# Kernel tuning notes

Hardware: AMD Instinct MI355X
Metric: run time of the kernel (lower is better)

The kernel has to match this reference:

```python
import jax, jax.numpy as jnp
import numpy as np

D, H = 64, 16
B, S = 4, 4096
PI = 3.1415  # constant used verbatim in the original code


def setup_inputs() -> dict:
    key = jax.random.key(0)
    ks = jax.random.split(key, 11)
    inp = {
        'query': jax.random.normal(ks[0], (B, S, D), dtype=jnp.float32),
        'key': jax.random.normal(ks[1], (B, S, D), dtype=jnp.float32),
        'value': jax.random.normal(ks[2], (B, S, D), dtype=jnp.float32),
        'attn_mask': jnp.zeros((1,), dtype=bool),
        # Linear weights stored as (in, out); y = x @ W + b
        'wq_w': jax.random.normal(ks[3], (D, D * H), dtype=jnp.float32) * 0.05,
        'wq_b': jnp.zeros((D * H,), dtype=jnp.float32),
        'wk_w': jax.random.normal(ks[4], (D, D * H), dtype=jnp.float32) * 0.05,
        'wk_b': jnp.zeros((D * H,), dtype=jnp.float32),
        'wv_w': jax.random.normal(ks[5], (D, D * H), dtype=jnp.float32) * 0.05,
        'wv_b': jnp.zeros((D * H,), dtype=jnp.float32),
        'dense_w': jax.random.normal(ks[6], (D * H, D), dtype=jnp.float32) * 0.05,
        'dense_b': jnp.zeros((D,), dtype=jnp.float32),
    }
    return inp


def reference(query, key, value, attn_mask, wq_w, wq_b, wk_w, wk_b, wv_w, wv_b, dense_w, dense_b):
    b, s, _ = query.shape
    # projections -> (B, S, H, D); einsum axis n = heads
    q = (query @ wq_w + wq_b).reshape(b, s, H, D)
    k = (key @ wk_w + wk_b).reshape(b, s, H, D)
    v = (value @ wv_w + wv_b).reshape(b, s, H, D)

    q = jax.nn.elu(q) + 1.0
    k = jax.nn.elu(k) + 1.0

    pos = PI * jnp.arange(s, dtype=query.dtype) / s  # (S,)
    qc_w = jnp.cos(pos)
    qs_w = jnp.sin(pos)
    kc_w = jnp.sin(pos)  # NB: original uses sin for k_cos too (faithful)
    ks_w = jnp.sin(pos)

    q_cos = q * qc_w[None, :, None, None]
    q_sin = q * qs_w[None, :, None, None]
    k_cos = k * kc_w[None, :, None, None]
    k_sin = k * ks_w[None, :, None, None]

    def lin_attn(qf, kf):
        kv = jnp.einsum('bsnx,bsnz->bnxz', kf, v)      # (B,H,D,D)
        return jnp.einsum('bsnx,bnxz->bsnz', qf, kv)   # (B,S,H,D)

    qkv = lin_attn(q, k)
    qkv_cos = lin_attn(q_cos, k_cos)
    qkv_sin = lin_attn(q_sin, k_sin)

    denom = 1.0 / (
        jnp.einsum('bsnd,bnd->bsn', q, k.sum(axis=1))
        + jnp.einsum('bsnd,bnd->bsn', q_cos, k_cos.sum(axis=1))
        + jnp.einsum('bsnd,bnd->bsn', q_sin, k_sin.sum(axis=1))
        + 1e-05
    )

    O = (qkv + qkv_cos + qkv_sin) * denom[..., None]   # (B,S,H,D)
    concat = O.reshape(b, s, H * D)
    return concat @ dense_w + dense_b
```

## Files before the change

kernel.cpp:

```cpp
#include <hip/hip_runtime.h>
#include <math.h>

#define BB 4
#define SS 4096
#define DD 64
#define HH 16
#define PI_C 3.1415f


typedef __attribute__((ext_vector_type(8))) short short8;
typedef __attribute__((ext_vector_type(4))) float f32x4;

#define MFMA(a, b, c) __builtin_amdgcn_mfma_f32_16x16x32_bf16(a, b, c, 0, 0, 0)

__device__ __forceinline__ short f2bf(float f) {
    union { float f; unsigned u; } v; v.f = f;
    unsigned r = v.u + 0x7FFFu + ((v.u >> 16) & 1u);
    return (short)(r >> 16);
}
__device__ __forceinline__ float bf2f(short s) {
    union { unsigned u; float f; } v;
    v.u = ((unsigned)(unsigned short)s) << 16;
    return v.f;
}
__device__ __forceinline__ short8 cvt8(float4 a, float4 b) {
    short8 r;
    r[0] = f2bf(a.x); r[1] = f2bf(a.y); r[2] = f2bf(a.z); r[3] = f2bf(a.w);
    r[4] = f2bf(b.x); r[5] = f2bf(b.y); r[6] = f2bf(b.z); r[7] = f2bf(b.w);
    return r;
}
__device__ __forceinline__ float elu1(float x) { return x > 0.f ? x + 1.f : __expf(x); }
__device__ __forceinline__ void st4(short* p, short a, short b, short c, short d) {
    union { uint2 u; short s[4]; } x;
    x.s[0] = a; x.s[1] = b; x.s[2] = c; x.s[3] = d;
    *reinterpret_cast<uint2*>(p) = x.u;
}

__global__ __launch_bounds__(256) void k_prep(
    const float* __restrict__ wq, const float* __restrict__ wk,
    const float* __restrict__ wv, const float* __restrict__ wd,
    short* __restrict__ dst)
{
    const int h = blockIdx.x, y = blockIdx.y, t = threadIdx.x;
    const float* src = (y == 0) ? wq : (y == 1) ? wk : (y == 2) ? wv : wd;
    const int rs = (y < 3) ? 1024 : 64;
    const size_t srcbase = (y < 3) ? (size_t)(h * 64) : (size_t)(h * 4096);
    short* dm = dst + (size_t)y * 65536 + (size_t)h * 4096;
#pragma unroll
    for (int j = 0; j < 4; ++j) {
        int idx = j * 1024 + t * 4;
        int r = idx >> 6, c = idx & 63;
        float4 v = *reinterpret_cast<const float4*>(src + (size_t)r * rs + srcbase + c);
        dm[(c + 0) * 64 + r] = f2bf(v.x);
        dm[(c + 1) * 64 + r] = f2bf(v.y);
        dm[(c + 2) * 64 + r] = f2bf(v.z);
        dm[(c + 3) * 64 + r] = f2bf(v.w);
    }
}

__global__ __launch_bounds__(256, 2) void k_phase1(
    const float* __restrict__ key, const float* __restrict__ value,
    const float* __restrict__ wk_b, const float* __restrict__ wv_b,
    const short* __restrict__ wkTb, const short* __restrict__ wvTb,
    float* __restrict__ pkv, float* __restrict__ pkvs,
    float* __restrict__ pks)
{
    const int chunk = blockIdx.x, h = blockIdx.y, b = blockIdx.z;
    const int t = threadIdx.x, w = t >> 6, l = t & 63;
    const int lane15 = l & 15, q8 = (l >> 4) * 8, q4 = (l >> 4) * 4;

    __shared__ short kT[2][64 * 72], vT[2][64 * 72], vsT[2][64 * 72];
    __shared__ float ssin[512];
    __shared__ float sbk[64], sbv[64];
    __shared__ float sred[512];

    short8 bkf[2][4], bvf[2][4];
    {
        const short* wkh = wkTb + (size_t)h * 4096;
        const short* wvh = wvTb + (size_t)h * 4096;
#pragma unroll
        for (int kss = 0; kss < 2; ++kss)
#pragma unroll
            for (int nt = 0; nt < 4; ++nt) {
                bkf[kss][nt] = *reinterpret_cast<const short8*>(wkh + (nt * 16 + lane15) * 64 + kss * 32 + q8);
                bvf[kss][nt] = *reinterpret_cast<const short8*>(wvh + (nt * 16 + lane15) * 64 + kss * 32 + q8);
            }
    }
    ssin[t]       = __sinf(PI_C * (float)(chunk * 512 + t)       * (1.f / 4096.f));
    ssin[t + 256] = __sinf(PI_C * (float)(chunk * 512 + t + 256) * (1.f / 4096.f));
    if (t < 64) sbk[t] = wk_b[h * 64 + t];
    else if (t < 128) sbv[t - 64] = wv_b[h * 64 + (t - 64)];

    float4 kf0, kf1, kf2, kf3, vf0, vf1, vf2, vf3;
    {
        const size_t g = ((size_t)b * SS + chunk * 512 + w * 16 + lane15) * 64 + q8;
        kf0 = *reinterpret_cast<const float4*>(key + g);
        kf1 = *reinterpret_cast<const float4*>(key + g + 4);
        kf2 = *reinterpret_cast<const float4*>(key + g + 32);
        kf3 = *reinterpret_cast<const float4*>(key + g + 36);
        vf0 = *reinterpret_cast<const float4*>(value + g);
        vf1 = *reinterpret_cast<const float4*>(value + g + 4);
        vf2 = *reinterpret_cast<const float4*>(value + g + 32);
        vf3 = *reinterpret_cast<const float4*>(value + g + 36);
    }

    f32x4 ckv[4], ckvs[4];
#pragma unroll
    for (int i = 0; i < 4; ++i) {
        ckv[i]  = (f32x4){0.f, 0.f, 0.f, 0.f};
        ckvs[i] = (f32x4){0.f, 0.f, 0.f, 0.f};
    }
    float aks = 0.f, akss = 0.f;

    auto proj_store = [&](int buf, int sbase) {
        f32x4 ckp[4], cvp[4];
#pragma unroll
        for (int i = 0; i < 4; ++i) {
            ckp[i] = (f32x4){0.f, 0.f, 0.f, 0.f};
            cvp[i] = (f32x4){0.f, 0.f, 0.f, 0.f};
        }
        short8 ak0 = cvt8(kf0, kf1), ak1 = cvt8(kf2, kf3);
        short8 av0 = cvt8(vf0, vf1), av1 = cvt8(vf2, vf3);
#pragma unroll
        for (int nt = 0; nt < 4; ++nt) {
            ckp[nt] = MFMA(ak0, bkf[0][nt], ckp[nt]);
            cvp[nt] = MFMA(av0, bvf[0][nt], cvp[nt]);
            ckp[nt] = MFMA(ak1, bkf[1][nt], ckp[nt]);
            cvp[nt] = MFMA(av1, bvf[1][nt], cvp[nt]);
        }
        const int srel = w * 16 + q4;
#pragma unroll
        for (int nt = 0; nt < 4; ++nt) {
            const int x = nt * 16 + lane15;
            const float bk = sbk[x], bv = sbv[x];
            short ek[4], ev[4], es[4];
#pragma unroll
            for (int r = 0; r < 4; ++r) {
                float kk = elu1(ckp[nt][r] + bk);
                float vv = cvp[nt][r] + bv;
                ek[r] = f2bf(kk);
                ev[r] = f2bf(vv);
                es[r] = f2bf(vv * ssin[sbase + srel + r]);
            }
            st4(&kT [buf][x * 72 + srel], ek[0], ek[1], ek[2], ek[3]);
            st4(&vT [buf][x * 72 + srel], ev[0], ev[1], ev[2], ev[3]);
            st4(&vsT[buf][x * 72 + srel], es[0], es[1], es[2], es[3]);
        }
    };

    __syncthreads();
    proj_store(0, 0);
    __syncthreads();

#pragma unroll 1
    for (int it = 0; it < 8; ++it) {
        const int cur = it & 1;
        if (it < 7) {
            const size_t g = ((size_t)b * SS + chunk * 512 + (it + 1) * 64 + w * 16 + lane15) * 64 + q8;
            kf0 = *reinterpret_cast<const float4*>(key + g);
            kf1 = *reinterpret_cast<const float4*>(key + g + 4);
            kf2 = *reinterpret_cast<const float4*>(key + g + 32);
            kf3 = *reinterpret_cast<const float4*>(key + g + 36);
            vf0 = *reinterpret_cast<const float4*>(value + g);
            vf1 = *reinterpret_cast<const float4*>(value + g + 4);
            vf2 = *reinterpret_cast<const float4*>(value + g + 32);
            vf3 = *reinterpret_cast<const float4*>(value + g + 36);
        }
#pragma unroll
        for (int kstep = 0; kstep < 2; ++kstep) {
            const int so = kstep * 32;
            short8 aV  = *reinterpret_cast<const short8*>(&vT [cur][(w * 16 + lane15) * 72 + so + q8]);
            short8 aVS = *reinterpret_cast<const short8*>(&vsT[cur][(w * 16 + lane15) * 72 + so + q8]);
#pragma unroll
            for (int nt = 0; nt < 4; ++nt) {
                short8 bK = *reinterpret_cast<const short8*>(&kT[cur][(nt * 16 + lane15) * 72 + so + q8]);
                ckv[nt]  = MFMA(aV,  bK, ckv[nt]);
                ckvs[nt] = MFMA(aVS, bK, ckvs[nt]);
            }
        }
        {
            const int sbase = it * 64;
            short8 k0 = *reinterpret_cast<const short8*>(&kT[cur][l * 72 + w * 16]);
            short8 k1 = *reinterpret_cast<const short8*>(&kT[cur][l * 72 + w * 16 + 8]);
#pragma unroll
            for (int e = 0; e < 8; ++e) {
                float fa = bf2f(k0[e]), fb = bf2f(k1[e]);
                aks  += fa + fb;
                akss += fa * ssin[sbase + w * 16 + e] + fb * ssin[sbase + w * 16 + 8 + e];
            }
        }
        if (it < 7) proj_store(cur ^ 1, (it + 1) * 64);
        __syncthreads();
    }

    const int bh = b * HH + h;
    const size_t pbase = ((size_t)(chunk * 64) + bh) * 4096;
#pragma unroll
    for (int nt = 0; nt < 4; ++nt) {
        const int x = nt * 16 + lane15;
#pragma unroll
        for (int r = 0; r < 4; ++r) {
            const int z = w * 16 + q4 + r;
            pkv [pbase + z * 64 + x] = ckv[nt][r];
            pkvs[pbase + z * 64 + x] = ckvs[nt][r];
        }
    }
    sred[t] = aks; sred[256 + t] = akss;
    __syncthreads();
    if (t < 64) {
        pks[((size_t)(chunk * 64) + bh) * 128 + t] =
            sred[t] + sred[64 + t] + sred[128 + t] + sred[192 + t];
    } else if (t < 128) {
        int tt = t - 64;
        pks[((size_t)(chunk * 64) + bh) * 128 + t] =
            sred[256 + tt] + sred[320 + tt] + sred[384 + tt] + sred[448 + tt];
    }
}

__global__ __launch_bounds__(256) void k_reduce(
    const float* __restrict__ pkv, const float* __restrict__ pkvs,
    const float* __restrict__ pks,
    short* __restrict__ kvb, short* __restrict__ kvsb,
    float* __restrict__ ksums)
{
    const int blk = blockIdx.x, t = threadIdx.x;
    if (blk < 512) {
        const float* src = (blk < 256) ? pkv : pkvs;
        short* dst = (blk < 256) ? kvb : kvsb;
        const int o4 = (blk & 255) * 256 + t;
        float4 s = make_float4(0.f, 0.f, 0.f, 0.f);
#pragma unroll
        for (int c = 0; c < 8; ++c) {
            float4 v = reinterpret_cast<const float4*>(src + (size_t)c * 262144)[o4];
            s.x += v.x; s.y += v.y; s.z += v.z; s.w += v.w;
        }
        st4(dst + (size_t)o4 * 4, f2bf(s.x), f2bf(s.y), f2bf(s.z), f2bf(s.w));
    } else {
        const int g = (blk - 512) * 256 + t;
        float4 s = make_float4(0.f, 0.f, 0.f, 0.f);
#pragma unroll
        for (int c = 0; c < 8; ++c) {
            float4 v = reinterpret_cast<const float4*>(pks + (size_t)c * 8192)[g];
            s.x += v.x; s.y += v.y; s.z += v.z; s.w += v.w;
        }
        reinterpret_cast<float4*>(ksums)[g] = s;
    }
}

__global__ __launch_bounds__(256, 2) void k_phase2(
    const float* __restrict__ query, const float* __restrict__ wq_b,
    const short* __restrict__ wqTb,
    const short* __restrict__ kvb, const short* __restrict__ kvsb,
    const float* __restrict__ ksums,
    const short* __restrict__ wdTb, const float* __restrict__ dense_b,
    float* __restrict__ out)
{
    const int st = blockIdx.x, b = blockIdx.y;
    const int s0 = st * 32;
    const int t = threadIdx.x, w = t >> 6, l = t & 63;
    const int lane15 = l & 15, q8 = (l >> 4) * 8, q4 = (l >> 4) * 4;

    __shared__ __align__(16) char smem[34816];
    __shared__ float scc[32];
    short* sqin = reinterpret_cast<short*>(smem);
    short* sqp  = reinterpret_cast<short*>(smem) + 2304 * (1 + w);
    short* sOw  = reinterpret_cast<short*>(smem) + 2304 * 5 + 1152 * w;

    {
        const int row = t >> 3, c8 = (t & 7) * 8;
        const float* qp = query + ((size_t)b * SS + s0 + row) * 64 + c8;
        float4 f0 = *reinterpret_cast<const float4*>(qp);
        float4 f1 = *reinterpret_cast<const float4*>(qp + 4);
        *reinterpret_cast<short8*>(&sqin[row * 72 + c8]) = cvt8(f0, f1);
    }
    if (t < 32) {
        float p = PI_C * (float)(s0 + t) * (1.f / 4096.f);
        scc[t] = __cosf(p) + __sinf(p);
    }
    f32x4 cd[2][4];
#pragma unroll
    for (int rt = 0; rt < 2; ++rt)
#pragma unroll
        for (int nt = 0; nt < 4; ++nt) cd[rt][nt] = (f32x4){0.f, 0.f, 0.f, 0.f};
    __syncthreads();

    short8 aq[2][2];
#pragma unroll
    for (int rt = 0; rt < 2; ++rt)
#pragma unroll
        for (int kss = 0; kss < 2; ++kss)
            aq[rt][kss] = *reinterpret_cast<const short8*>(&sqin[(rt * 16 + lane15) * 72 + kss * 32 + q8]);
    const float ccs0 = scc[lane15], ccs1 = scc[16 + lane15];
    const int drow = l >> 1, dxh = (l & 1) * 32;
    const float ccr = scc[drow];

#pragma unroll 1
    for (int i = 0; i < 4; ++i) {
        const int h = (i << 2) | w;
        const size_t bh = (size_t)(b * HH + h);
        const short* wqh = wqTb + (size_t)h * 4096;
        const short* wdh = wdTb + (size_t)h * 4096;
        const short* kv1 = kvb  + bh * 4096;
        const short* kv2 = kvsb + bh * 4096;

        f32x4 cq[2][4];
#pragma unroll
        for (int rt = 0; rt < 2; ++rt)
#pragma unroll
            for (int nt = 0; nt < 4; ++nt) cq[rt][nt] = (f32x4){0.f, 0.f, 0.f, 0.f};
#pragma unroll
        for (int nt = 0; nt < 4; ++nt) {
            short8 b0 = *reinterpret_cast<const short8*>(wqh + (nt * 16 + lane15) * 64 + q8);
            short8 b1 = *reinterpret_cast<const short8*>(wqh + (nt * 16 + lane15) * 64 + 32 + q8);
            cq[0][nt] = MFMA(b0, aq[0][0], cq[0][nt]);
            cq[1][nt] = MFMA(b0, aq[1][0], cq[1][nt]);
            cq[0][nt] = MFMA(b1, aq[0][1], cq[0][nt]);
            cq[1][nt] = MFMA(b1, aq[1][1], cq[1][nt]);
        }
#pragma unroll
        for (int nt = 0; nt < 4; ++nt) {
            float4 bq = *reinterpret_cast<const float4*>(wq_b + h * 64 + nt * 16 + q4);
#pragma unroll
            for (int rt = 0; rt < 2; ++rt) {
                short e0 = f2bf(elu1(cq[rt][nt][0] + bq.x));
                short e1 = f2bf(elu1(cq[rt][nt][1] + bq.y));
                short e2 = f2bf(elu1(cq[rt][nt][2] + bq.z));
                short e3 = f2bf(elu1(cq[rt][nt][3] + bq.w));
                st4(&sqp[(rt * 16 + lane15) * 72 + nt * 16 + q4], e0, e1, e2, e3);
            }
        }

        float invs0, invs1;
        {
            const float* kp = ksums + bh * 128 + dxh;
            float4 A[8], Bv[8];
#pragma unroll
            for (int j = 0; j < 8; ++j) {
                A[j]  = *reinterpret_cast<const float4*>(kp + j * 4);
                Bv[j] = *reinterpret_cast<const float4*>(kp + 64 + j * 4);
            }
            short8 qr[4];
#pragma unroll
            for (int e = 0; e < 4; ++e)
                qr[e] = *reinterpret_cast<const short8*>(&sqp[drow * 72 + dxh + e * 8]);
            float dsum = 0.f;
#pragma unroll
            for (int j4 = 0; j4 < 8; ++j4)
#pragma unroll
                for (int e4 = 0; e4 < 4; ++e4)
                    dsum += bf2f(qr[j4 >> 1][(j4 & 1) * 4 + e4]) * (A[j4][e4] + ccr * Bv[j4][e4]);
            dsum += __shfl_xor(dsum, 1);
            float invd = 1.f / (dsum + 1e-5f);
            invs0 = __shfl(invd, lane15 * 2);
            invs1 = __shfl(invd, (16 + lane15) * 2);
        }

        short8 qf[2][2];
#pragma unroll
        for (int rt = 0; rt < 2; ++rt)
#pragma unroll
            for (int kss = 0; kss < 2; ++kss)
                qf[rt][kss] = *reinterpret_cast<const short8*>(&sqp[(rt * 16 + lane15) * 72 + kss * 32 + q8]);
        f32x4 cv1[2][4], cv2[2][4];
#pragma unroll
        for (int rt = 0; rt < 2; ++rt)
#pragma unroll
            for (int nt = 0; nt < 4; ++nt) {
                cv1[rt][nt] = (f32x4){0.f, 0.f, 0.f, 0.f};
                cv2[rt][nt] = (f32x4){0.f, 0.f, 0.f, 0.f};
            }
#pragma unroll
        for (int nt = 0; nt < 4; ++nt) {
            const short* a1 = kv1 + (nt * 16 + lane15) * 64;
            const short* a2 = kv2 + (nt * 16 + lane15) * 64;
            short8 f10 = *reinterpret_cast<const short8*>(a1 + q8);
            short8 f11 = *reinterpret_cast<const short8*>(a1 + 32 + q8);
            short8 f20 = *reinterpret_cast<const short8*>(a2 + q8);
            short8 f21 = *reinterpret_cast<const short8*>(a2 + 32 + q8);
#pragma unroll
            for (int rt = 0; rt < 2; ++rt) {
                cv1[rt][nt] = MFMA(f10, qf[rt][0], cv1[rt][nt]);
                cv1[rt][nt] = MFMA(f11, qf[rt][1], cv1[rt][nt]);
                cv2[rt][nt] = MFMA(f20, qf[rt][0], cv2[rt][nt]);
                cv2[rt][nt] = MFMA(f21, qf[rt][1], cv2[rt][nt]);
            }
        }
        short8 wdf[4][2];
#pragma unroll
        for (int nt = 0; nt < 4; ++nt)
#pragma unroll
            for (int kss = 0; kss < 2; ++kss)
                wdf[nt][kss] = *reinterpret_cast<const short8*>(wdh + (nt * 16 + lane15) * 64 + kss * 32 + q8);

#pragma unroll
        for (int rt = 0; rt < 2; ++rt) {
            const float ccsr = rt ? ccs1 : ccs0;
            const float invr = rt ? invs1 : invs0;
#pragma unroll
            for (int nt = 0; nt < 4; ++nt) {
                short e0 = f2bf((cv1[rt][nt][0] + ccsr * cv2[rt][nt][0]) * invr);
                short e1 = f2bf((cv1[rt][nt][1] + ccsr * cv2[rt][nt][1]) * invr);
                short e2 = f2bf((cv1[rt][nt][2] + ccsr * cv2[rt][nt][2]) * invr);
                short e3 = f2bf((cv1[rt][nt][3] + ccsr * cv2[rt][nt][3]) * invr);
                st4(&sOw[lane15 * 72 + nt * 16 + q4], e0, e1, e2, e3);
            }
            short8 of0 = *reinterpret_cast<const short8*>(&sOw[lane15 * 72 + q8]);
            short8 of1 = *reinterpret_cast<const short8*>(&sOw[lane15 * 72 + 32 + q8]);
#pragma unroll
            for (int nt = 0; nt < 4; ++nt) {
                cd[rt][nt] = MFMA(of0, wdf[nt][0], cd[rt][nt]);
                cd[rt][nt] = MFMA(of1, wdf[nt][1], cd[rt][nt]);
            }
        }
    }

    __syncthreads();
    {
        float* red = reinterpret_cast<float*>(smem) + 2176 * w;
#pragma unroll
        for (int rt = 0; rt < 2; ++rt)
#pragma unroll
            for (int nt = 0; nt < 4; ++nt)
#pragma unroll
                for (int r = 0; r < 4; ++r)
                    red[(rt * 16 + q4 + r) * 68 + nt * 16 + lane15] = cd[rt][nt][r];
    }
    __syncthreads();
    {
        const int row = t >> 3, c8 = (t & 7) * 8;
        float4 sa = make_float4(0.f, 0.f, 0.f, 0.f);
        float4 sb = make_float4(0.f, 0.f, 0.f, 0.f);
#pragma unroll
        for (int ww = 0; ww < 4; ++ww) {
            const float* red = reinterpret_cast<const float*>(smem) + 2176 * ww;
            float4 v0 = *reinterpret_cast<const float4*>(red + row * 68 + c8);
            float4 v1 = *reinterpret_cast<const float4*>(red + row * 68 + c8 + 4);
            sa.x += v0.x; sa.y += v0.y; sa.z += v0.z; sa.w += v0.w;
            sb.x += v1.x; sb.y += v1.y; sb.z += v1.z; sb.w += v1.w;
        }
        float4 d0 = *reinterpret_cast<const float4*>(dense_b + c8);
        float4 d1 = *reinterpret_cast<const float4*>(dense_b + c8 + 4);
        sa.x += d0.x; sa.y += d0.y; sa.z += d0.z; sa.w += d0.w;
        sb.x += d1.x; sb.y += d1.y; sb.z += d1.z; sb.w += d1.w;
        float* op = out + ((size_t)b * SS + s0 + row) * 64 + c8;
        *reinterpret_cast<float4*>(op)     = sa;
        *reinterpret_cast<float4*>(op + 4) = sb;
    }
}

extern "C" void kernel_launch(void* const* d_in, const int* in_sizes, int n_in,
                              void* d_out, int out_size, void* d_ws, size_t ws_size,
                              hipStream_t stream) {
    const float* query   = (const float*)d_in[0];
    const float* key     = (const float*)d_in[1];
    const float* value   = (const float*)d_in[2];
    const float* wq_w    = (const float*)d_in[4];
    const float* wq_b    = (const float*)d_in[5];
    const float* wk_w    = (const float*)d_in[6];
    const float* wk_b    = (const float*)d_in[7];
    const float* wv_w    = (const float*)d_in[8];
    const float* wv_b    = (const float*)d_in[9];
    const float* dense_w = (const float*)d_in[10];
    const float* dense_b = (const float*)d_in[11];
    float* out = (float*)d_out;

    char* ws = (char*)d_ws;
    float* pkv   = (float*)(ws);
    float* pkvs  = (float*)(ws + 8388608);
    float* pks   = (float*)(ws + 16777216);
    short* kvb   = (short*)(ws + 17039360);
    short* kvsb  = (short*)(ws + 17563648);
    float* ksums = (float*)(ws + 18087936);
    short* wT    = (short*)(ws + 18120704);
    short* wqTb  = wT;
    short* wkTb  = wT + 65536;
    short* wvTb  = wT + 131072;
    short* wdTb  = wT + 196608;

    hipLaunchKernelGGL(k_prep, dim3(16, 4), dim3(256), 0, stream,
                       wq_w, wk_w, wv_w, dense_w, wT);
    hipLaunchKernelGGL(k_phase1, dim3(8, HH, BB), dim3(256), 0, stream,
                       key, value, wk_b, wv_b, wkTb, wvTb, pkv, pkvs, pks);
    hipLaunchKernelGGL(k_reduce, dim3(520), dim3(256), 0, stream,
                       pkv, pkvs, pks, kvb, kvsb, ksums);
    hipLaunchKernelGGL(k_phase2, dim3(128, BB), dim3(256), 0, stream,
                       query, wq_b, wqTb, kvb, kvsb, ksums, wdTb, dense_b, out);
}
```

Before: 152.6 us.

## Fuse four kernel launches into one cooperative kernel with grid syncs

Merges the weight-prep, KV-accumulation, reduction and output phases into a single cooperative kernel of 512 blocks, separated by grid-wide barriers. This removes three kernel-launch boundaries and their drain/ramp gaps. If the cooperative launch fails, the code falls back to the original four launches. Grid syncs carry their own cost, and the fused kernel is restricted to 2 blocks per CU at 256 threads with a large shared-memory footprint, which may limit occupancy.

```diff
diff --git a/kernel.cpp b/kernel.cpp
--- a/kernel.cpp
+++ b/kernel.cpp
@@ -1,5 +1,8 @@
 #include <hip/hip_runtime.h>
+#include <hip/hip_cooperative_groups.h>
 #include <math.h>
+
+namespace cg = cooperative_groups;
 
 #define BB 4
 #define SS 4096
@@ -36,6 +39,428 @@
     *reinterpret_cast<uint2*>(p) = x.u;
 }
 
+__global__ __launch_bounds__(256, 2) void k_fused(
+    const float* __restrict__ query, const float* __restrict__ key,
+    const float* __restrict__ value,
+    const float* __restrict__ wq_w, const float* __restrict__ wk_w,
+    const float* __restrict__ wv_w, const float* __restrict__ dense_w,
+    const float* __restrict__ wq_b, const float* __restrict__ wk_b,
+    const float* __restrict__ wv_b, const float* __restrict__ dense_b,
+    float* __restrict__ pkv, float* __restrict__ pkvs, float* __restrict__ pks,
+    short* __restrict__ kvb, short* __restrict__ kvsb, float* __restrict__ ksums,
+    short* __restrict__ wT, float* __restrict__ out)
+{
+    const int blk = blockIdx.x, t = threadIdx.x;
+    const int w = t >> 6, l = t & 63;
+    const int lane15 = l & 15, q8 = (l >> 4) * 8, q4 = (l >> 4) * 4;
+
+    __shared__ __align__(16) char usmem[59904];
+    cg::grid_group grid = cg::this_grid();
+
+    const short* wqTb = wT;
+    const short* wkTb = wT + 65536;
+    const short* wvTb = wT + 131072;
+    const short* wdTb = wT + 196608;
+
+    if (blk < 64) {
+        const int h = blk & 15, y = blk >> 4;
+        const float* src = (y == 0) ? wq_w : (y == 1) ? wk_w : (y == 2) ? wv_w : dense_w;
+        const int rs = (y < 3) ? 1024 : 64;
+        const size_t srcbase = (y < 3) ? (size_t)(h * 64) : (size_t)(h * 4096);
+        short* dm = wT + (size_t)y * 65536 + (size_t)h * 4096;
+#pragma unroll
+        for (int j = 0; j < 4; ++j) {
+            int idx = j * 1024 + t * 4;
+            int r = idx >> 6, c = idx & 63;
+            float4 v = *reinterpret_cast<const float4*>(src + (size_t)r * rs + srcbase + c);
+            dm[(c + 0) * 64 + r] = f2bf(v.x);
+            dm[(c + 1) * 64 + r] = f2bf(v.y);
+            dm[(c + 2) * 64 + r] = f2bf(v.z);
+            dm[(c + 3) * 64 + r] = f2bf(v.w);
+        }
+    }
+    grid.sync();
+
+    {
+        const int chunk = blk & 7, h = (blk >> 3) & 15, b = blk >> 7;
+
+        short* kTb  = reinterpret_cast<short*>(usmem);
+        short* vTb  = reinterpret_cast<short*>(usmem + 18432);
+        short* vsTb = reinterpret_cast<short*>(usmem + 36864);
+        float* ssin = reinterpret_cast<float*>(usmem + 55296);
+        float* sbk  = reinterpret_cast<float*>(usmem + 57344);
+        float* sbv  = reinterpret_cast<float*>(usmem + 57600);
+        float* sred = reinterpret_cast<float*>(usmem + 57856);
+
+        short8 bkf[2][4], bvf[2][4];
+        {
+            const short* wkh = wkTb + (size_t)h * 4096;
+            const short* wvh = wvTb + (size_t)h * 4096;
+#pragma unroll
+            for (int kss = 0; kss < 2; ++kss)
+#pragma unroll
+                for (int nt = 0; nt < 4; ++nt) {
+                    bkf[kss][nt] = *reinterpret_cast<const short8*>(wkh + (nt * 16 + lane15) * 64 + kss * 32 + q8);
+                    bvf[kss][nt] = *reinterpret_cast<const short8*>(wvh + (nt * 16 + lane15) * 64 + kss * 32 + q8);
+                }
+        }
+        ssin[t]       = __sinf(PI_C * (float)(chunk * 512 + t)       * (1.f / 4096.f));
+        ssin[t + 256] = __sinf(PI_C * (float)(chunk * 512 + t + 256) * (1.f / 4096.f));
+        if (t < 64) sbk[t] = wk_b[h * 64 + t];
+        else if (t < 128) sbv[t - 64] = wv_b[h * 64 + (t - 64)];
+
+        float4 kf0, kf1, kf2, kf3, vf0, vf1, vf2, vf3;
+        {
+            const size_t g = ((size_t)b * SS + chunk * 512 + w * 16 + lane15) * 64 + q8;
+            kf0 = *reinterpret_cast<const float4*>(key + g);
+            kf1 = *reinterpret_cast<const float4*>(key + g + 4);
+            kf2 = *reinterpret_cast<const float4*>(key + g + 32);
+            kf3 = *reinterpret_cast<const float4*>(key + g + 36);
+            vf0 = *reinterpret_cast<const float4*>(value + g);
+            vf1 = *reinterpret_cast<const float4*>(value + g + 4);
+            vf2 = *reinterpret_cast<const float4*>(value + g + 32);
+            vf3 = *reinterpret_cast<const float4*>(value + g + 36);
+        }
+
+        f32x4 ckv[4], ckvs[4];
+#pragma unroll
+        for (int i = 0; i < 4; ++i) {
+            ckv[i]  = (f32x4){0.f, 0.f, 0.f, 0.f};
+            ckvs[i] = (f32x4){0.f, 0.f, 0.f, 0.f};
+        }
+        float aks = 0.f, akss = 0.f;
+
+        auto proj_store = [&](int buf, int sbase) {
+            f32x4 ckp[4], cvp[4];
+#pragma unroll
+            for (int i = 0; i < 4; ++i) {
+                ckp[i] = (f32x4){0.f, 0.f, 0.f, 0.f};
+                cvp[i] = (f32x4){0.f, 0.f, 0.f, 0.f};
+            }
+            short8 ak0 = cvt8(kf0, kf1), ak1 = cvt8(kf2, kf3);
+            short8 av0 = cvt8(vf0, vf1), av1 = cvt8(vf2, vf3);
+#pragma unroll
+            for (int nt = 0; nt < 4; ++nt) {
+                ckp[nt] = MFMA(ak0, bkf[0][nt], ckp[nt]);
+                cvp[nt] = MFMA(av0, bvf[0][nt], cvp[nt]);
+                ckp[nt] = MFMA(ak1, bkf[1][nt], ckp[nt]);
+                cvp[nt] = MFMA(av1, bvf[1][nt], cvp[nt]);
+            }
+            const int srel = w * 16 + q4;
+            short* kTc  = kTb  + buf * 4608;
+            short* vTc  = vTb  + buf * 4608;
+            short* vsTc = vsTb + buf * 4608;
+#pragma unroll
+            for (int nt = 0; nt < 4; ++nt) {
+                const int x = nt * 16 + lane15;
+                const float bk = sbk[x], bv = sbv[x];
+                short ek[4], ev[4], es[4];
+#pragma unroll
+                for (int r = 0; r < 4; ++r) {
+                    float kk = elu1(ckp[nt][r] + bk);
+                    float vv = cvp[nt][r] + bv;
+                    ek[r] = f2bf(kk);
+                    ev[r] = f2bf(vv);
+                    es[r] = f2bf(vv * ssin[sbase + srel + r]);
+                }
+                st4(&kTc [x * 72 + srel], ek[0], ek[1], ek[2], ek[3]);
+                st4(&vTc [x * 72 + srel], ev[0], ev[1], ev[2], ev[3]);
+                st4(&vsTc[x * 72 + srel], es[0], es[1], es[2], es[3]);
+            }
+        };
+
+        __syncthreads();
+        proj_store(0, 0);
+        __syncthreads();
+
+#pragma unroll 1
+        for (int it = 0; it < 8; ++it) {
+            const int cur = it & 1;
+            if (it < 7) {
+                const size_t g = ((size_t)b * SS + chunk * 512 + (it + 1) * 64 + w * 16 + lane15) * 64 + q8;
+                kf0 = *reinterpret_cast<const float4*>(key + g);
+                kf1 = *reinterpret_cast<const float4*>(key + g + 4);
+                kf2 = *reinterpret_cast<const float4*>(key + g + 32);
+                kf3 = *reinterpret_cast<const float4*>(key + g + 36);
+                vf0 = *reinterpret_cast<const float4*>(value + g);
+                vf1 = *reinterpret_cast<const float4*>(value + g + 4);
+                vf2 = *reinterpret_cast<const float4*>(value + g + 32);
+                vf3 = *reinterpret_cast<const float4*>(value + g + 36);
+            }
+            const short* kTc  = kTb  + cur * 4608;
+            const short* vTc  = vTb  + cur * 4608;
+            const short* vsTc = vsTb + cur * 4608;
+#pragma unroll
+            for (int kstep = 0; kstep < 2; ++kstep) {
+                const int so = kstep * 32;
+                short8 aV  = *reinterpret_cast<const short8*>(&vTc [(w * 16 + lane15) * 72 + so + q8]);
+                short8 aVS = *reinterpret_cast<const short8*>(&vsTc[(w * 16 + lane15) * 72 + so + q8]);
+#pragma unroll
+                for (int nt = 0; nt < 4; ++nt) {
+                    short8 bK = *reinterpret_cast<const short8*>(&kTc[(nt * 16 + lane15) * 72 + so + q8]);
+                    ckv[nt]  = MFMA(aV,  bK, ckv[nt]);
+                    ckvs[nt] = MFMA(aVS, bK, ckvs[nt]);
+                }
+            }
+            {
+                const int sbase = it * 64;
+                short8 k0 = *reinterpret_cast<const short8*>(&kTc[l * 72 + w * 16]);
+                short8 k1 = *reinterpret_cast<const short8*>(&kTc[l * 72 + w * 16 + 8]);
+#pragma unroll
+                for (int e = 0; e < 8; ++e) {
+                    float fa = bf2f(k0[e]), fb = bf2f(k1[e]);
+                    aks  += fa + fb;
+                    akss += fa * ssin[sbase + w * 16 + e] + fb * ssin[sbase + w * 16 + 8 + e];
+                }
+            }
+            if (it < 7) proj_store(cur ^ 1, (it + 1) * 64);
+            __syncthreads();
+        }
+
+        const int bh = b * HH + h;
+        const size_t pbase = ((size_t)(chunk * 64) + bh) * 4096;
+#pragma unroll
+        for (int nt = 0; nt < 4; ++nt) {
+            const int x = nt * 16 + lane15;
+#pragma unroll
+            for (int r = 0; r < 4; ++r) {
+                const int z = w * 16 + q4 + r;
+                pkv [pbase + z * 64 + x] = ckv[nt][r];
+                pkvs[pbase + z * 64 + x] = ckvs[nt][r];
+            }
+        }
+        sred[t] = aks; sred[256 + t] = akss;
+        __syncthreads();
+        if (t < 64) {
+            pks[((size_t)(chunk * 64) + bh) * 128 + t] =
+                sred[t] + sred[64 + t] + sred[128 + t] + sred[192 + t];
+        } else if (t < 128) {
+            int tt = t - 64;
+            pks[((size_t)(chunk * 64) + bh) * 128 + t] =
+                sred[256 + tt] + sred[320 + tt] + sred[384 + tt] + sred[448 + tt];
+        }
+    }
+    grid.sync();
+
+    {
+        const int gidx = blk * 256 + t;
+        {
+            const bool first = gidx < 65536;
+            const float* src = first ? pkv : pkvs;
+            short* dst = first ? kvb : kvsb;
+            const int o4 = gidx & 65535;
+            float4 s = make_float4(0.f, 0.f, 0.f, 0.f);
+#pragma unroll
+            for (int c = 0; c < 8; ++c) {
+                float4 v = reinterpret_cast<const float4*>(src + (size_t)c * 262144)[o4];
+                s.x += v.x; s.y += v.y; s.z += v.z; s.w += v.w;
+            }
+            st4(dst + (size_t)o4 * 4, f2bf(s.x), f2bf(s.y), f2bf(s.z), f2bf(s.w));
+        }
+        if (gidx < 2048) {
+            float4 s = make_float4(0.f, 0.f, 0.f, 0.f);
+#pragma unroll
+            for (int c = 0; c < 8; ++c) {
+                float4 v = reinterpret_cast<const float4*>(pks + (size_t)c * 8192)[gidx];
+                s.x += v.x; s.y += v.y; s.z += v.z; s.w += v.w;
+            }
+            reinterpret_cast<float4*>(ksums)[gidx] = s;
+        }
+    }
+    grid.sync();
+
+    {
+        const int st = blk & 127, b = blk >> 7;
+        const int s0 = st * 32;
+
+        short* sqin = reinterpret_cast<short*>(usmem);
+        short* sqp  = reinterpret_cast<short*>(usmem) + 2304 * (1 + w);
+        short* sOw  = reinterpret_cast<short*>(usmem) + 2304 * 5 + 1152 * w;
+        float* scc  = reinterpret_cast<float*>(usmem + 34816);
+
+        {
+            const int row = t >> 3, c8 = (t & 7) * 8;
+            const float* qp = query + ((size_t)b * SS + s0 + row) * 64 + c8;
+            float4 f0 = *reinterpret_cast<const float4*>(qp);
+            float4 f1 = *reinterpret_cast<const float4*>(qp + 4);
+            *reinterpret_cast<short8*>(&sqin[row * 72 + c8]) = cvt8(f0, f1);
+        }
+        if (t < 32) {
+            float p = PI_C * (float)(s0 + t) * (1.f / 4096.f);
+            scc[t] = __cosf(p) + __sinf(p);
+        }
+        f32x4 cd[2][4];
+#pragma unroll
+        for (int rt = 0; rt < 2; ++rt)
+#pragma unroll
+            for (int nt = 0; nt < 4; ++nt) cd[rt][nt] = (f32x4){0.f, 0.f, 0.f, 0.f};
+        __syncthreads();
+
+        short8 aq[2][2];
+#pragma unroll
+        for (int rt = 0; rt < 2; ++rt)
+#pragma unroll
+            for (int kss = 0; kss < 2; ++kss)
+                aq[rt][kss] = *reinterpret_cast<const short8*>(&sqin[(rt * 16 + lane15) * 72 + kss * 32 + q8]);
+        const float ccs0 = scc[lane15], ccs1 = scc[16 + lane15];
+        const int drow = l >> 1, dxh = (l & 1) * 32;
+        const float ccr = scc[drow];
+
+#pragma unroll 1
+        for (int i = 0; i < 4; ++i) {
+            const int h = (i << 2) | w;
+            const size_t bh = (size_t)(b * HH + h);
+            const short* wqh = wqTb + (size_t)h * 4096;
+            const short* wdh = wdTb + (size_t)h * 4096;
+            const short* kv1 = kvb  + bh * 4096;
+            const short* kv2 = kvsb + bh * 4096;
+
+            f32x4 cq[2][4];
+#pragma unroll
+            for (int rt = 0; rt < 2; ++rt)
+#pragma unroll
+                for (int nt = 0; nt < 4; ++nt) cq[rt][nt] = (f32x4){0.f, 0.f, 0.f, 0.f};
+#pragma unroll
+            for (int nt = 0; nt < 4; ++nt) {
+                short8 b0 = *reinterpret_cast<const short8*>(wqh + (nt * 16 + lane15) * 64 + q8);
+                short8 b1 = *reinterpret_cast<const short8*>(wqh + (nt * 16 + lane15) * 64 + 32 + q8);
+                cq[0][nt] = MFMA(b0, aq[0][0], cq[0][nt]);
+                cq[1][nt] = MFMA(b0, aq[1][0], cq[1][nt]);
+                cq[0][nt] = MFMA(b1, aq[0][1], cq[0][nt]);
+                cq[1][nt] = MFMA(b1, aq[1][1], cq[1][nt]);
+            }
+#pragma unroll
+            for (int nt = 0; nt < 4; ++nt) {
+                float4 bq = *reinterpret_cast<const float4*>(wq_b + h * 64 + nt * 16 + q4);
+#pragma unroll
+                for (int rt = 0; rt < 2; ++rt) {
+                    short e0 = f2bf(elu1(cq[rt][nt][0] + bq.x));
+                    short e1 = f2bf(elu1(cq[rt][nt][1] + bq.y));
+                    short e2 = f2bf(elu1(cq[rt][nt][2] + bq.z));
+                    short e3 = f2bf(elu1(cq[rt][nt][3] + bq.w));
+                    st4(&sqp[(rt * 16 + lane15) * 72 + nt * 16 + q4], e0, e1, e2, e3);
+                }
+            }
+
+            float invs0, invs1;
+            {
+                const float* kp = ksums + bh * 128 + dxh;
+                float4 A[8], Bv[8];
+#pragma unroll
+                for (int j = 0; j < 8; ++j) {
+                    A[j]  = *reinterpret_cast<const float4*>(kp + j * 4);
+                    Bv[j] = *reinterpret_cast<const float4*>(kp + 64 + j * 4);
+                }
+                short8 qr[4];
+#pragma unroll
+                for (int e = 0; e < 4; ++e)
+                    qr[e] = *reinterpret_cast<const short8*>(&sqp[drow * 72 + dxh + e * 8]);
+                float dsum = 0.f;
+#pragma unroll
+                for (int j4 = 0; j4 < 8; ++j4)
+#pragma unroll
+                    for (int e4 = 0; e4 < 4; ++e4)
+                        dsum += bf2f(qr[j4 >> 1][(j4 & 1) * 4 + e4]) * (A[j4][e4] + ccr * Bv[j4][e4]);
+                dsum += __shfl_xor(dsum, 1);
+                float invd = 1.f / (dsum + 1e-5f);
+                invs0 = __shfl(invd, lane15 * 2);
+                invs1 = __shfl(invd, (16 + lane15) * 2);
+            }
+
+            short8 qf[2][2];
+#pragma unroll
+            for (int rt = 0; rt < 2; ++rt)
+#pragma unroll
+                for (int kss = 0; kss < 2; ++kss)
+                    qf[rt][kss] = *reinterpret_cast<const short8*>(&sqp[(rt * 16 + lane15) * 72 + kss * 32 + q8]);
+            f32x4 cv1[2][4], cv2[2][4];
+#pragma unroll
+            for (int rt = 0; rt < 2; ++rt)
+#pragma unroll
+                for (int nt = 0; nt < 4; ++nt) {
+                    cv1[rt][nt] = (f32x4){0.f, 0.f, 0.f, 0.f};
+                    cv2[rt][nt] = (f32x4){0.f, 0.f, 0.f, 0.f};
+                }
+#pragma unroll
+            for (int nt = 0; nt < 4; ++nt) {
+                const short* a1 = kv1 + (nt * 16 + lane15) * 64;
+                const short* a2 = kv2 + (nt * 16 + lane15) * 64;
+                short8 f10 = *reinterpret_cast<const short8*>(a1 + q8);
+                short8 f11 = *reinterpret_cast<const short8*>(a1 + 32 + q8);
+                short8 f20 = *reinterpret_cast<const short8*>(a2 + q8);
+                short8 f21 = *reinterpret_cast<const short8*>(a2 + 32 + q8);
+#pragma unroll
+                for (int rt = 0; rt < 2; ++rt) {
+                    cv1[rt][nt] = MFMA(f10, qf[rt][0], cv1[rt][nt]);
+                    cv1[rt][nt] = MFMA(f11, qf[rt][1], cv1[rt][nt]);
+                    cv2[rt][nt] = MFMA(f20, qf[rt][0], cv2[rt][nt]);
+                    cv2[rt][nt] = MFMA(f21, qf[rt][1], cv2[rt][nt]);
+                }
+            }
+            short8 wdf[4][2];
+#pragma unroll
+            for (int nt = 0; nt < 4; ++nt)
+#pragma unroll
+                for (int kss = 0; kss < 2; ++kss)
+                    wdf[nt][kss] = *reinterpret_cast<const short8*>(wdh + (nt * 16 + lane15) * 64 + kss * 32 + q8);
+
+#pragma unroll
+            for (int rt = 0; rt < 2; ++rt) {
+                const float ccsr = rt ? ccs1 : ccs0;
+                const float invr = rt ? invs1 : invs0;
+#pragma unroll
+                for (int nt = 0; nt < 4; ++nt) {
+                    short e0 = f2bf((cv1[rt][nt][0] + ccsr * cv2[rt][nt][0]) * invr);
+                    short e1 = f2bf((cv1[rt][nt][1] + ccsr * cv2[rt][nt][1]) * invr);
+                    short e2 = f2bf((cv1[rt][nt][2] + ccsr * cv2[rt][nt][2]) * invr);
+                    short e3 = f2bf((cv1[rt][nt][3] + ccsr * cv2[rt][nt][3]) * invr);
+                    st4(&sOw[lane15 * 72 + nt * 16 + q4], e0, e1, e2, e3);
+                }
+                short8 of0 = *reinterpret_cast<const short8*>(&sOw[lane15 * 72 + q8]);
+                short8 of1 = *reinterpret_cast<const short8*>(&sOw[lane15 * 72 + 32 + q8]);
+#pragma unroll
+                for (int nt = 0; nt < 4; ++nt) {
+                    cd[rt][nt] = MFMA(of0, wdf[nt][0], cd[rt][nt]);
+                    cd[rt][nt] = MFMA(of1, wdf[nt][1], cd[rt][nt]);
+                }
+            }
+        }
+
+        __syncthreads();
+        {
+            float* red = reinterpret_cast<float*>(usmem) + 2176 * w;
+#pragma unroll
+            for (int rt = 0; rt < 2; ++rt)
+#pragma unroll
+                for (int nt = 0; nt < 4; ++nt)
+#pragma unroll
+                    for (int r = 0; r < 4; ++r)
+                        red[(rt * 16 + q4 + r) * 68 + nt * 16 + lane15] = cd[rt][nt][r];
+        }
+        __syncthreads();
+        {
+            const int row = t >> 3, c8 = (t & 7) * 8;
+            float4 sa = make_float4(0.f, 0.f, 0.f, 0.f);
+            float4 sb = make_float4(0.f, 0.f, 0.f, 0.f);
+#pragma unroll
+            for (int ww = 0; ww < 4; ++ww) {
+                const float* red = reinterpret_cast<const float*>(usmem) + 2176 * ww;
+                float4 v0 = *reinterpret_cast<const float4*>(red + row * 68 + c8);
+                float4 v1 = *reinterpret_cast<const float4*>(red + row * 68 + c8 + 4);
+                sa.x += v0.x; sa.y += v0.y; sa.z += v0.z; sa.w += v0.w;
+                sb.x += v1.x; sb.y += v1.y; sb.z += v1.z; sb.w += v1.w;
+            }
+            float4 d0 = *reinterpret_cast<const float4*>(dense_b + c8);
+            float4 d1 = *reinterpret_cast<const float4*>(dense_b + c8 + 4);
+            sa.x += d0.x; sa.y += d0.y; sa.z += d0.z; sa.w += d0.w;
+            sb.x += d1.x; sb.y += d1.y; sb.z += d1.z; sb.w += d1.w;
+            float* op = out + ((size_t)b * SS + s0 + row) * 64 + c8;
+            *reinterpret_cast<float4*>(op)     = sa;
+            *reinterpret_cast<float4*>(op + 4) = sb;
+        }
+    }
+}
+
 __global__ __launch_bounds__(256) void k_prep(
     const float* __restrict__ wq, const float* __restrict__ wk,
     const float* __restrict__ wv, const float* __restrict__ wd,
@@ -477,12 +902,24 @@
     short* wvTb  = wT + 131072;
     short* wdTb  = wT + 196608;
 
-    hipLaunchKernelGGL(k_prep, dim3(16, 4), dim3(256), 0, stream,
-                       wq_w, wk_w, wv_w, dense_w, wT);
-    hipLaunchKernelGGL(k_phase1, dim3(8, HH, BB), dim3(256), 0, stream,
-                       key, value, wk_b, wv_b, wkTb, wvTb, pkv, pkvs, pks);
-    hipLaunchKernelGGL(k_reduce, dim3(520), dim3(256), 0, stream,
-                       pkv, pkvs, pks, kvb, kvsb, ksums);
-    hipLaunchKernelGGL(k_phase2, dim3(128, BB), dim3(256), 0, stream,
-                       query, wq_b, wqTb, kvb, kvsb, ksums, wdTb, dense_b, out);
+    void* kargs[] = {
+        (void*)&query, (void*)&key, (void*)&value,
+        (void*)&wq_w, (void*)&wk_w, (void*)&wv_w, (void*)&dense_w,
+        (void*)&wq_b, (void*)&wk_b, (void*)&wv_b, (void*)&dense_b,
+        (void*)&pkv, (void*)&pkvs, (void*)&pks,
+        (void*)&kvb, (void*)&kvsb, (void*)&ksums, (void*)&wT, (void*)&out
+    };
+    hipError_t ce = hipLaunchCooperativeKernel(
+        (void*)k_fused, dim3(512), dim3(256), kargs, 0, stream);
+
+    if (ce != hipSuccess) {
+        hipLaunchKernelGGL(k_prep, dim3(16, 4), dim3(256), 0, stream,
+                           wq_w, wk_w, wv_w, dense_w, wT);
+        hipLaunchKernelGGL(k_phase1, dim3(8, HH, BB), dim3(256), 0, stream,
+                           key, value, wk_b, wv_b, wkTb, wvTb, pkv, pkvs, pks);
+        hipLaunchKernelGGL(k_reduce, dim3(520), dim3(256), 0, stream,
+                           pkv, pkvs, pks, kvb, kvsb, ksums);
+        hipLaunchKernelGGL(k_phase2, dim3(128, BB), dim3(256), 0, stream,
+                           query, wq_b, wqTb, kvb, kvsb, ksums, wdTb, dense_b, out);
+    }
 }
```

Result: slower. 352.2 us (+130.7%).

## Fuse weight prep and chunk reduction into phase1 with last-block atomic reduce

Applied to the files above, without the earlier changes.

Merges the weight-transpose kernel and the partial-sum reduction kernel into phase1, cutting two kernel launches. Each phase1 block now converts its head's K/V weights to bf16 in shared memory itself, and extra blocks convert the Q and dense weights. The last of the 8 chunk blocks per (batch, head), found with an atomic counter, sums the partials. The counter lives in the output buffer, which is zeroed with a memset before phase2 overwrites it. This adds a memset launch and redundant per-block weight conversion, and depends on correct fence ordering.

```diff
diff --git a/kernel.cpp b/kernel.cpp
--- a/kernel.cpp
+++ b/kernel.cpp
@@ -36,60 +36,48 @@
     *reinterpret_cast<uint2*>(p) = x.u;
 }
 
-__global__ __launch_bounds__(256) void k_prep(
-    const float* __restrict__ wq, const float* __restrict__ wk,
-    const float* __restrict__ wv, const float* __restrict__ wd,
-    short* __restrict__ dst)
-{
-    const int h = blockIdx.x, y = blockIdx.y, t = threadIdx.x;
-    const float* src = (y == 0) ? wq : (y == 1) ? wk : (y == 2) ? wv : wd;
-    const int rs = (y < 3) ? 1024 : 64;
-    const size_t srcbase = (y < 3) ? (size_t)(h * 64) : (size_t)(h * 4096);
-    short* dm = dst + (size_t)y * 65536 + (size_t)h * 4096;
-#pragma unroll
-    for (int j = 0; j < 4; ++j) {
-        int idx = j * 1024 + t * 4;
-        int r = idx >> 6, c = idx & 63;
-        float4 v = *reinterpret_cast<const float4*>(src + (size_t)r * rs + srcbase + c);
-        dm[(c + 0) * 64 + r] = f2bf(v.x);
-        dm[(c + 1) * 64 + r] = f2bf(v.y);
-        dm[(c + 2) * 64 + r] = f2bf(v.z);
-        dm[(c + 3) * 64 + r] = f2bf(v.w);
-    }
-}
-
-__global__ __launch_bounds__(256, 2) void k_phase1(
+__global__ __launch_bounds__(256, 2) void k_phase1x(
     const float* __restrict__ key, const float* __restrict__ value,
     const float* __restrict__ wk_b, const float* __restrict__ wv_b,
-    const short* __restrict__ wkTb, const short* __restrict__ wvTb,
+    const float* __restrict__ wk_w, const float* __restrict__ wv_w,
+    const float* __restrict__ wq_w, const float* __restrict__ wd_w,
     float* __restrict__ pkv, float* __restrict__ pkvs,
-    float* __restrict__ pks)
+    float* __restrict__ pks,
+    short* __restrict__ kvb, short* __restrict__ kvsb,
+    float* __restrict__ ksums,
+    short* __restrict__ wT, int* __restrict__ cnt)
 {
-    const int chunk = blockIdx.x, h = blockIdx.y, b = blockIdx.z;
-    const int t = threadIdx.x, w = t >> 6, l = t & 63;
-    const int lane15 = l & 15, q8 = (l >> 4) * 8, q4 = (l >> 4) * 4;
+    const int blk = blockIdx.x, t = threadIdx.x;
 
     __shared__ short kT[2][64 * 72], vT[2][64 * 72], vsT[2][64 * 72];
     __shared__ float ssin[512];
     __shared__ float sbk[64], sbv[64];
     __shared__ float sred[512];
 
-    short8 bkf[2][4], bvf[2][4];
-    {
-        const short* wkh = wkTb + (size_t)h * 4096;
-        const short* wvh = wvTb + (size_t)h * 4096;
-#pragma unroll
-        for (int kss = 0; kss < 2; ++kss)
-#pragma unroll
-            for (int nt = 0; nt < 4; ++nt) {
-                bkf[kss][nt] = *reinterpret_cast<const short8*>(wkh + (nt * 16 + lane15) * 64 + kss * 32 + q8);
-                bvf[kss][nt] = *reinterpret_cast<const short8*>(wvh + (nt * 16 + lane15) * 64 + kss * 32 + q8);
-            }
-    }
-    ssin[t]       = __sinf(PI_C * (float)(chunk * 512 + t)       * (1.f / 4096.f));
-    ssin[t + 256] = __sinf(PI_C * (float)(chunk * 512 + t + 256) * (1.f / 4096.f));
-    if (t < 64) sbk[t] = wk_b[h * 64 + t];
-    else if (t < 128) sbv[t - 64] = wv_b[h * 64 + (t - 64)];
+    if (blk >= 512) {
+        const int pb = blk - 512;
+        const int h = pb & 15;
+        const bool isQ = (pb < 16);
+        const float* src = isQ ? wq_w : wd_w;
+        const int rs = isQ ? 1024 : 64;
+        const size_t srcbase = isQ ? (size_t)(h * 64) : (size_t)(h * 4096);
+        short* dm = wT + (isQ ? (size_t)0 : (size_t)3 * 65536) + (size_t)h * 4096;
+#pragma unroll
+        for (int j = 0; j < 4; ++j) {
+            int idx = j * 1024 + t * 4;
+            int r = idx >> 6, c = idx & 63;
+            float4 v = *reinterpret_cast<const float4*>(src + (size_t)r * rs + srcbase + c);
+            dm[(c + 0) * 64 + r] = f2bf(v.x);
+            dm[(c + 1) * 64 + r] = f2bf(v.y);
+            dm[(c + 2) * 64 + r] = f2bf(v.z);
+            dm[(c + 3) * 64 + r] = f2bf(v.w);
+        }
+        return;
+    }
+
+    const int chunk = blk & 7, h = (blk >> 3) & 15, b = blk >> 7;
+    const int w = t >> 6, l = t & 63;
+    const int lane15 = l & 15, q8 = (l >> 4) * 8, q4 = (l >> 4) * 4;
 
     float4 kf0, kf1, kf2, kf3, vf0, vf1, vf2, vf3;
     {
@@ -104,6 +92,42 @@
         vf3 = *reinterpret_cast<const float4*>(value + g + 36);
     }
 
+    short* wkL = &kT[0][0];
+    short* wvL = &kT[1][0];
+    {
+        const int r = t >> 2, c0 = (t & 3) * 16;
+        const float* pkw = wk_w + (size_t)r * 1024 + h * 64 + c0;
+        const float* pvw = wv_w + (size_t)r * 1024 + h * 64 + c0;
+#pragma unroll
+        for (int q = 0; q < 4; ++q) {
+            float4 a = *reinterpret_cast<const float4*>(pkw + q * 4);
+            float4 v = *reinterpret_cast<const float4*>(pvw + q * 4);
+            wkL[(c0 + q * 4 + 0) * 72 + r] = f2bf(a.x);
+            wkL[(c0 + q * 4 + 1) * 72 + r] = f2bf(a.y);
+            wkL[(c0 + q * 4 + 2) * 72 + r] = f2bf(a.z);
+            wkL[(c0 + q * 4 + 3) * 72 + r] = f2bf(a.w);
+            wvL[(c0 + q * 4 + 0) * 72 + r] = f2bf(v.x);
+            wvL[(c0 + q * 4 + 1) * 72 + r] = f2bf(v.y);
+            wvL[(c0 + q * 4 + 2) * 72 + r] = f2bf(v.z);
+            wvL[(c0 + q * 4 + 3) * 72 + r] = f2bf(v.w);
+        }
+    }
+    ssin[t]       = __sinf(PI_C * (float)(chunk * 512 + t)       * (1.f / 4096.f));
+    ssin[t + 256] = __sinf(PI_C * (float)(chunk * 512 + t + 256) * (1.f / 4096.f));
+    if (t < 64) sbk[t] = wk_b[h * 64 + t];
+    else if (t < 128) sbv[t - 64] = wv_b[h * 64 + (t - 64)];
+    __syncthreads();
+
+    short8 bkf[2][4], bvf[2][4];
+#pragma unroll
+    for (int kss = 0; kss < 2; ++kss)
+#pragma unroll
+        for (int nt = 0; nt < 4; ++nt) {
+            bkf[kss][nt] = *reinterpret_cast<const short8*>(&wkL[(nt * 16 + lane15) * 72 + kss * 32 + q8]);
+            bvf[kss][nt] = *reinterpret_cast<const short8*>(&wvL[(nt * 16 + lane15) * 72 + kss * 32 + q8]);
+        }
+    __syncthreads();
+
     f32x4 ckv[4], ckvs[4];
 #pragma unroll
     for (int i = 0; i < 4; ++i) {
@@ -148,7 +172,6 @@
         }
     };
 
-    __syncthreads();
     proj_store(0, 0);
     __syncthreads();
 
@@ -215,35 +238,33 @@
         pks[((size_t)(chunk * 64) + bh) * 128 + t] =
             sred[256 + tt] + sred[320 + tt] + sred[384 + tt] + sred[448 + tt];
     }
-}
-
-__global__ __launch_bounds__(256) void k_reduce(
-    const float* __restrict__ pkv, const float* __restrict__ pkvs,
-    const float* __restrict__ pks,
-    short* __restrict__ kvb, short* __restrict__ kvsb,
-    float* __restrict__ ksums)
-{
-    const int blk = blockIdx.x, t = threadIdx.x;
-    if (blk < 512) {
-        const float* src = (blk < 256) ? pkv : pkvs;
-        short* dst = (blk < 256) ? kvb : kvsb;
-        const int o4 = (blk & 255) * 256 + t;
-        float4 s = make_float4(0.f, 0.f, 0.f, 0.f);
-#pragma unroll
-        for (int c = 0; c < 8; ++c) {
-            float4 v = reinterpret_cast<const float4*>(src + (size_t)c * 262144)[o4];
-            s.x += v.x; s.y += v.y; s.z += v.z; s.w += v.w;
-        }
-        st4(dst + (size_t)o4 * 4, f2bf(s.x), f2bf(s.y), f2bf(s.z), f2bf(s.w));
-    } else {
-        const int g = (blk - 512) * 256 + t;
-        float4 s = make_float4(0.f, 0.f, 0.f, 0.f);
-#pragma unroll
-        for (int c = 0; c < 8; ++c) {
-            float4 v = reinterpret_cast<const float4*>(pks + (size_t)c * 8192)[g];
-            s.x += v.x; s.y += v.y; s.z += v.z; s.w += v.w;
-        }
-        reinterpret_cast<float4*>(ksums)[g] = s;
+
+    __threadfence();
+    __syncthreads();
+    if (t == 0) sred[0] = (float)atomicAdd(&cnt[bh], 1);
+    __syncthreads();
+    if ((int)sred[0] == 7) {
+        __threadfence();
+        for (int o4 = t; o4 < 1024; o4 += 256) {
+            float4 s1 = make_float4(0.f, 0.f, 0.f, 0.f);
+            float4 s2 = make_float4(0.f, 0.f, 0.f, 0.f);
+#pragma unroll
+            for (int c = 0; c < 8; ++c) {
+                const size_t pb4 = ((size_t)(c * 64) + bh) * 1024 + o4;
+                float4 v1 = reinterpret_cast<const float4*>(pkv)[pb4];
+                float4 v2 = reinterpret_cast<const float4*>(pkvs)[pb4];
+                s1.x += v1.x; s1.y += v1.y; s1.z += v1.z; s1.w += v1.w;
+                s2.x += v2.x; s2.y += v2.y; s2.z += v2.z; s2.w += v2.w;
+            }
+            st4(kvb  + (size_t)bh * 4096 + o4 * 4, f2bf(s1.x), f2bf(s1.y), f2bf(s1.z), f2bf(s1.w));
+            st4(kvsb + (size_t)bh * 4096 + o4 * 4, f2bf(s2.x), f2bf(s2.y), f2bf(s2.z), f2bf(s2.w));
+        }
+        if (t < 128) {
+            float s = 0.f;
+#pragma unroll
+            for (int c = 0; c < 8; ++c) s += pks[((size_t)(c * 64) + bh) * 128 + t];
+            ksums[(size_t)bh * 128 + t] = s;
+        }
     }
 }
 
@@ -473,16 +494,14 @@
     float* ksums = (float*)(ws + 18087936);
     short* wT    = (short*)(ws + 18120704);
     short* wqTb  = wT;
-    short* wkTb  = wT + 65536;
-    short* wvTb  = wT + 131072;
     short* wdTb  = wT + 196608;
 
-    hipLaunchKernelGGL(k_prep, dim3(16, 4), dim3(256), 0, stream,
-                       wq_w, wk_w, wv_w, dense_w, wT);
-    hipLaunchKernelGGL(k_phase1, dim3(8, HH, BB), dim3(256), 0, stream,
-                       key, value, wk_b, wv_b, wkTb, wvTb, pkv, pkvs, pks);
-    hipLaunchKernelGGL(k_reduce, dim3(520), dim3(256), 0, stream,
-                       pkv, pkvs, pks, kvb, kvsb, ksums);
+    int* cnt = (int*)out;
+    hipMemsetAsync(out, 0, 256, stream);
+
+    hipLaunchKernelGGL(k_phase1x, dim3(544), dim3(256), 0, stream,
+                       key, value, wk_b, wv_b, wk_w, wv_w, wq_w, dense_w,
+                       pkv, pkvs, pks, kvb, kvsb, ksums, wT, cnt);
     hipLaunchKernelGGL(k_phase2, dim3(128, BB), dim3(256), 0, stream,
                        query, wq_b, wqTb, kvb, kvsb, ksums, wdTb, dense_b, out);
 }
```

Result: slower. 238.2 us (+56.1%).
